# Performance work log

Measured on AMD Instinct MI355X. Metric: run time of the kernel, lower is better.

## Reference

```python
import jax, jax.numpy as jnp
import numpy as np

ALPHA = 0.2       # leakyrelu negative slope
NEG_INF = -9e15   # mask fill value from the torch code
D_OUT = 64


def setup_inputs() -> dict:
    key = jax.random.key(0)
    k1, k2, k3, k4 = jax.random.split(key, 4)
    N, D_IN = 8192, 512
    h = jax.random.normal(k1, (N, D_IN), dtype=jnp.float32)
    W = jax.random.normal(k2, (D_IN, D_OUT), dtype=jnp.float32) * (1.0 / np.sqrt(D_IN))
    a = jax.random.normal(k3, (2 * D_OUT, 1), dtype=jnp.float32) * 0.1
    randomadj = jax.random.randint(k4, (N, N), 0, 2, dtype=jnp.int32)
    return {"h": h, "W": W, "a": a, "randomadj": randomadj}


def reference(h, W, a, randomadj):
    # Wh: [N, D_OUT]
    Wh = h @ W
    # additive attention scores: e[i,j] = leakyrelu(Wh[i]@a1 + Wh[j]@a2)
    Wh1 = Wh @ a[:D_OUT, :]   # [N, 1]
    Wh2 = Wh @ a[D_OUT:, :]   # [N, 1]
    e = jax.nn.leaky_relu(Wh1 + Wh2.T, negative_slope=ALPHA)  # [N, N]
    masked = jnp.where(randomadj > 0, e, NEG_INF)
    attention = jax.nn.softmax(masked, axis=1)  # dropout skipped (eval mode)
    h_prime = attention @ Wh                    # [N, D_OUT]
    return jax.nn.elu(h_prime)                  # concat=True path
```

## Files before the change

kernel.cpp:

```cpp
#include <hip/hip_runtime.h>
#include <stdint.h>


constexpr int NN = 8192;
constexpr int DIN = 512;
constexpr int DOUT = 64;

typedef __attribute__((ext_vector_type(4))) float f32x4;
typedef __attribute__((ext_vector_type(8))) short short8;
typedef int int32x4 __attribute__((ext_vector_type(4)));

__device__ __forceinline__ unsigned short f2bf(float x) {
  union { float f; uint32_t u; } v; v.f = x;
  return (unsigned short)((v.u + 0x7fffu + ((v.u >> 16) & 1u)) >> 16);
}

__device__ __forceinline__ int frag_byte(int c, int d) {
  int g = (c >> 2) & 3;
  int i = (c & 3) | (((c >> 4) & 1) << 2);
  return ((c >> 5) << 12) | ((d >> 4) << 10) | (((g << 4) | (d & 15)) << 4) | (i << 1);
}

__global__ __launch_bounds__(256) void k1_wh(
    const float* __restrict__ h, const float* __restrict__ W,
    const float* __restrict__ a, unsigned short* __restrict__ whb,
    float* __restrict__ wh1, float* __restrict__ wh2) {
  const int t = threadIdx.x, w = t >> 6, l = t & 63;
  const int r = blockIdx.x * 4 + w;
  const int q = l >> 4, cg = l & 15;
  const float* hr = h + (size_t)r * DIN + q * 128;
  const float* Wp = W + (size_t)(q * 128) * DOUT + cg * 4;
  float ax = 0.f, ay = 0.f, az = 0.f, aw = 0.f;
#pragma unroll 4
  for (int kk = 0; kk < 32; ++kk) {
    float4 h4 = *(const float4*)(hr + kk * 4);
    const float* wr = Wp + (size_t)kk * 4 * DOUT;
    float4 w0 = *(const float4*)(wr);
    float4 w1 = *(const float4*)(wr + DOUT);
    float4 w2 = *(const float4*)(wr + 2 * DOUT);
    float4 w3 = *(const float4*)(wr + 3 * DOUT);
    ax = fmaf(h4.x, w0.x, ax); ay = fmaf(h4.x, w0.y, ay); az = fmaf(h4.x, w0.z, az); aw = fmaf(h4.x, w0.w, aw);
    ax = fmaf(h4.y, w1.x, ax); ay = fmaf(h4.y, w1.y, ay); az = fmaf(h4.y, w1.z, az); aw = fmaf(h4.y, w1.w, aw);
    ax = fmaf(h4.z, w2.x, ax); ay = fmaf(h4.z, w2.y, ay); az = fmaf(h4.z, w2.z, az); aw = fmaf(h4.z, w2.w, aw);
    ax = fmaf(h4.w, w3.x, ax); ay = fmaf(h4.w, w3.y, ay); az = fmaf(h4.w, w3.z, az); aw = fmaf(h4.w, w3.w, aw);
  }
  ax += __shfl_xor(ax, 16, 64); ax += __shfl_xor(ax, 32, 64);
  ay += __shfl_xor(ay, 16, 64); ay += __shfl_xor(ay, 32, 64);
  az += __shfl_xor(az, 16, 64); az += __shfl_xor(az, 32, 64);
  aw += __shfl_xor(aw, 16, 64); aw += __shfl_xor(aw, 32, 64);
  float4 a1v = *(const float4*)(a + cg * 4);
  float4 a2v = *(const float4*)(a + DOUT + cg * 4);
  float d1 = ax * a1v.x + ay * a1v.y + az * a1v.z + aw * a1v.w;
  float d2 = ax * a2v.x + ay * a2v.y + az * a2v.z + aw * a2v.w;
#pragma unroll
  for (int m = 8; m >= 1; m >>= 1) { d1 += __shfl_xor(d1, m, 64); d2 += __shfl_xor(d2, m, 64); }
  if (l == 0) { wh1[r] = d1; wh2[r] = d2; }
  if (l < 16) {
    whb[frag_byte(r, cg * 4 + 0) >> 1] = f2bf(ax);
    whb[frag_byte(r, cg * 4 + 1) >> 1] = f2bf(ay);
    whb[frag_byte(r, cg * 4 + 2) >> 1] = f2bf(az);
    whb[frag_byte(r, cg * 4 + 3) >> 1] = f2bf(aw);
  }
}

struct KRegs {
  int32x4 a0, a1;
  float4 f0, f1;
  uint4 v0, v1, v2, v3;
};

__global__ __launch_bounds__(256, 2) void k2_attn(
    const int* __restrict__ adj, const unsigned short* __restrict__ whb,
    const float* __restrict__ wh1, const float* __restrict__ wh2,
    float* __restrict__ out) {
  __shared__ float accs[4][16][64];
  __shared__ float lsum[4][16];
  const int t = threadIdx.x, w = t >> 6, l = t & 63;
  const int r0 = blockIdx.x * 16;
  const int row = l & 15, g = l >> 4;
  const float wh1r = wh1[r0 + row];
  const int jb = w * 2048 + 4 * g;
  const int32x4* adjp = (const int32x4*)(adj + (size_t)(r0 + row) * NN + jb);
  const float4* w2p = (const float4*)(wh2 + jb);
  const uint4* vp = (const uint4*)whb + (size_t)w * 64 * 256 + l;
  f32x4 acc0 = {}, acc1 = {}, acc2 = {}, acc3 = {};
  float lacc = 0.f;

#define LOADC(R, c) do { \
    R.a0 = __builtin_nontemporal_load(adjp + (c) * 8); \
    R.a1 = __builtin_nontemporal_load(adjp + (c) * 8 + 4); \
    R.f0 = w2p[(c) * 8]; R.f1 = w2p[(c) * 8 + 4]; \
    R.v0 = vp[(c) * 256]; R.v1 = vp[(c) * 256 + 64]; \
    R.v2 = vp[(c) * 256 + 128]; R.v3 = vp[(c) * 256 + 192]; \
  } while (0)

#define SC(pv, av, fv) { float s_ = wh1r + (fv); s_ = fmaxf(s_, 0.2f * s_); \
                         float e_ = __expf(s_); pv = ((av) > 0) ? e_ : 0.f; }

#define COMP(R) do { \
    float p0, p1, p2, p3, p4, p5, p6, p7; \
    SC(p0, R.a0.x, R.f0.x) SC(p1, R.a0.y, R.f0.y) SC(p2, R.a0.z, R.f0.z) SC(p3, R.a0.w, R.f0.w) \
    SC(p4, R.a1.x, R.f1.x) SC(p5, R.a1.y, R.f1.y) SC(p6, R.a1.z, R.f1.z) SC(p7, R.a1.w, R.f1.w) \
    lacc += ((p0 + p1) + (p2 + p3)) + ((p4 + p5) + (p6 + p7)); \
    union { uint32_t u[4]; short8 s; } af; \
    af.u[0] = f2bf(p0) | ((uint32_t)f2bf(p1) << 16); \
    af.u[1] = f2bf(p2) | ((uint32_t)f2bf(p3) << 16); \
    af.u[2] = f2bf(p4) | ((uint32_t)f2bf(p5) << 16); \
    af.u[3] = f2bf(p6) | ((uint32_t)f2bf(p7) << 16); \
    union { uint4 q; short8 s; } b0, b1, b2, b3; \
    b0.q = R.v0; b1.q = R.v1; b2.q = R.v2; b3.q = R.v3; \
    acc0 = __builtin_amdgcn_mfma_f32_16x16x32_bf16(af.s, b0.s, acc0, 0, 0, 0); \
    acc1 = __builtin_amdgcn_mfma_f32_16x16x32_bf16(af.s, b1.s, acc1, 0, 0, 0); \
    acc2 = __builtin_amdgcn_mfma_f32_16x16x32_bf16(af.s, b2.s, acc2, 0, 0, 0); \
    acc3 = __builtin_amdgcn_mfma_f32_16x16x32_bf16(af.s, b3.s, acc3, 0, 0, 0); \
  } while (0)

  KRegs A, B;
  LOADC(A, 0);
  LOADC(B, 1);
  for (int c = 0; c + 2 < 64; c += 2) {
    COMP(A); LOADC(A, c + 2);
    COMP(B); LOADC(B, c + 3);
  }
  COMP(A);
  COMP(B);

  lacc += __shfl_xor(lacc, 16, 64);
  lacc += __shfl_xor(lacc, 32, 64);
  if (l < 16) lsum[w][l] = lacc;
  {
    const int rb = (l >> 4) * 4, cl = l & 15;
#define WACC(an, n) { accs[w][rb + 0][(n)*16 + cl] = an[0]; accs[w][rb + 1][(n)*16 + cl] = an[1]; \
                      accs[w][rb + 2][(n)*16 + cl] = an[2]; accs[w][rb + 3][(n)*16 + cl] = an[3]; }
    WACC(acc0, 0) WACC(acc1, 1) WACC(acc2, 2) WACC(acc3, 3)
#undef WACC
  }
  __syncthreads();
  {
    const int rr = t >> 4, dq = (t & 15) * 4;
    float4 s0 = *(const float4*)&accs[0][rr][dq];
    float4 s1 = *(const float4*)&accs[1][rr][dq];
    float4 s2 = *(const float4*)&accs[2][rr][dq];
    float4 s3 = *(const float4*)&accs[3][rr][dq];
    float L = (lsum[0][rr] + lsum[1][rr]) + (lsum[2][rr] + lsum[3][rr]);
    float inv = 1.0f / L;
    float4 o;
    float v;
    v = (s0.x + s1.x + s2.x + s3.x) * inv; o.x = v > 0.f ? v : __expf(v) - 1.f;
    v = (s0.y + s1.y + s2.y + s3.y) * inv; o.y = v > 0.f ? v : __expf(v) - 1.f;
    v = (s0.z + s1.z + s2.z + s3.z) * inv; o.z = v > 0.f ? v : __expf(v) - 1.f;
    v = (s0.w + s1.w + s2.w + s3.w) * inv; o.w = v > 0.f ? v : __expf(v) - 1.f;
    *(float4*)(out + (size_t)(r0 + rr) * DOUT + dq) = o;
  }
#undef LOADC
#undef SC
#undef COMP
}

extern "C" void kernel_launch(void* const* d_in, const int* in_sizes, int n_in,
                              void* d_out, int out_size, void* d_ws, size_t ws_size,
                              hipStream_t stream) {
  const float* h = (const float*)d_in[0];
  const float* W = (const float*)d_in[1];
  const float* a = (const float*)d_in[2];
  const int* adj = (const int*)d_in[3];
  float* out = (float*)d_out;
  char* ws = (char*)d_ws;
  unsigned short* whb = (unsigned short*)ws;
  float* wh1 = (float*)(ws + (1 << 20));
  float* wh2 = (float*)(ws + (1 << 20) + (32 << 10));
  k1_wh<<<NN / 4, 256, 0, stream>>>(h, W, a, whb, wh1, wh2);
  k2_attn<<<NN / 16, 256, 0, stream>>>(adj, whb, wh1, wh2, out);
}
```

Measured before the change: 433.3 us.

## Split attention columns across eight waves and reuse W across rows in projection

The attention kernel now uses 512-thread blocks, with each of 8 waves covering 1024 columns. Launch bounds are raised so more waves stay resident to hide the latency of streaming the adjacency matrix. The projection kernel computes four rows per wave so each W load is reused, and bf16 packing uses the library conversion intrinsic. The cost is more shared memory for the cross-wave reduction, and register pressure under the tighter launch bounds may cause spills.

```diff
diff --git a/kernel.cpp b/kernel.cpp
--- a/kernel.cpp
+++ b/kernel.cpp
@@ -1,4 +1,5 @@
 #include <hip/hip_runtime.h>
+#include <hip/hip_bf16.h>
 #include <stdint.h>
 
 
@@ -26,40 +27,55 @@
     const float* __restrict__ a, unsigned short* __restrict__ whb,
     float* __restrict__ wh1, float* __restrict__ wh2) {
   const int t = threadIdx.x, w = t >> 6, l = t & 63;
-  const int r = blockIdx.x * 4 + w;
+  const int r0 = blockIdx.x * 16 + w * 4;
   const int q = l >> 4, cg = l & 15;
-  const float* hr = h + (size_t)r * DIN + q * 128;
+  const float* h0 = h + (size_t)r0 * DIN + q * 128;
   const float* Wp = W + (size_t)(q * 128) * DOUT + cg * 4;
-  float ax = 0.f, ay = 0.f, az = 0.f, aw = 0.f;
+  f32x4 acc[4] = {};
 #pragma unroll 4
   for (int kk = 0; kk < 32; ++kk) {
-    float4 h4 = *(const float4*)(hr + kk * 4);
     const float* wr = Wp + (size_t)kk * 4 * DOUT;
     float4 w0 = *(const float4*)(wr);
     float4 w1 = *(const float4*)(wr + DOUT);
     float4 w2 = *(const float4*)(wr + 2 * DOUT);
     float4 w3 = *(const float4*)(wr + 3 * DOUT);
-    ax = fmaf(h4.x, w0.x, ax); ay = fmaf(h4.x, w0.y, ay); az = fmaf(h4.x, w0.z, az); aw = fmaf(h4.x, w0.w, aw);
-    ax = fmaf(h4.y, w1.x, ax); ay = fmaf(h4.y, w1.y, ay); az = fmaf(h4.y, w1.z, az); aw = fmaf(h4.y, w1.w, aw);
-    ax = fmaf(h4.z, w2.x, ax); ay = fmaf(h4.z, w2.y, ay); az = fmaf(h4.z, w2.z, az); aw = fmaf(h4.z, w2.w, aw);
-    ax = fmaf(h4.w, w3.x, ax); ay = fmaf(h4.w, w3.y, ay); az = fmaf(h4.w, w3.z, az); aw = fmaf(h4.w, w3.w, aw);
+#pragma unroll
+    for (int r = 0; r < 4; ++r) {
+      float4 h4 = *(const float4*)(h0 + (size_t)r * DIN + kk * 4);
+      acc[r][0] = fmaf(h4.x, w0.x, acc[r][0]); acc[r][1] = fmaf(h4.x, w0.y, acc[r][1]);
+      acc[r][2] = fmaf(h4.x, w0.z, acc[r][2]); acc[r][3] = fmaf(h4.x, w0.w, acc[r][3]);
+      acc[r][0] = fmaf(h4.y, w1.x, acc[r][0]); acc[r][1] = fmaf(h4.y, w1.y, acc[r][1]);
+      acc[r][2] = fmaf(h4.y, w1.z, acc[r][2]); acc[r][3] = fmaf(h4.y, w1.w, acc[r][3]);
+      acc[r][0] = fmaf(h4.z, w2.x, acc[r][0]); acc[r][1] = fmaf(h4.z, w2.y, acc[r][1]);
+      acc[r][2] = fmaf(h4.z, w2.z, acc[r][2]); acc[r][3] = fmaf(h4.z, w2.w, acc[r][3]);
+      acc[r][0] = fmaf(h4.w, w3.x, acc[r][0]); acc[r][1] = fmaf(h4.w, w3.y, acc[r][1]);
+      acc[r][2] = fmaf(h4.w, w3.z, acc[r][2]); acc[r][3] = fmaf(h4.w, w3.w, acc[r][3]);
+    }
   }
-  ax += __shfl_xor(ax, 16, 64); ax += __shfl_xor(ax, 32, 64);
-  ay += __shfl_xor(ay, 16, 64); ay += __shfl_xor(ay, 32, 64);
-  az += __shfl_xor(az, 16, 64); az += __shfl_xor(az, 32, 64);
-  aw += __shfl_xor(aw, 16, 64); aw += __shfl_xor(aw, 32, 64);
+#pragma unroll
+  for (int r = 0; r < 4; ++r)
+#pragma unroll
+    for (int cpt = 0; cpt < 4; ++cpt) {
+      float v = acc[r][cpt];
+      v += __shfl_xor(v, 16, 64);
+      v += __shfl_xor(v, 32, 64);
+      acc[r][cpt] = v;
+    }
   float4 a1v = *(const float4*)(a + cg * 4);
   float4 a2v = *(const float4*)(a + DOUT + cg * 4);
-  float d1 = ax * a1v.x + ay * a1v.y + az * a1v.z + aw * a1v.w;
-  float d2 = ax * a2v.x + ay * a2v.y + az * a2v.z + aw * a2v.w;
 #pragma unroll
-  for (int m = 8; m >= 1; m >>= 1) { d1 += __shfl_xor(d1, m, 64); d2 += __shfl_xor(d2, m, 64); }
-  if (l == 0) { wh1[r] = d1; wh2[r] = d2; }
-  if (l < 16) {
-    whb[frag_byte(r, cg * 4 + 0) >> 1] = f2bf(ax);
-    whb[frag_byte(r, cg * 4 + 1) >> 1] = f2bf(ay);
-    whb[frag_byte(r, cg * 4 + 2) >> 1] = f2bf(az);
-    whb[frag_byte(r, cg * 4 + 3) >> 1] = f2bf(aw);
+  for (int r = 0; r < 4; ++r) {
+    float d1 = acc[r][0] * a1v.x + acc[r][1] * a1v.y + acc[r][2] * a1v.z + acc[r][3] * a1v.w;
+    float d2 = acc[r][0] * a2v.x + acc[r][1] * a2v.y + acc[r][2] * a2v.z + acc[r][3] * a2v.w;
+#pragma unroll
+    for (int m = 8; m >= 1; m >>= 1) { d1 += __shfl_xor(d1, m, 64); d2 += __shfl_xor(d2, m, 64); }
+    if (l == 0) { wh1[r0 + r] = d1; wh2[r0 + r] = d2; }
+    if (l < 16) {
+      whb[frag_byte(r0 + r, cg * 4 + 0) >> 1] = f2bf(acc[r][0]);
+      whb[frag_byte(r0 + r, cg * 4 + 1) >> 1] = f2bf(acc[r][1]);
+      whb[frag_byte(r0 + r, cg * 4 + 2) >> 1] = f2bf(acc[r][2]);
+      whb[frag_byte(r0 + r, cg * 4 + 3) >> 1] = f2bf(acc[r][3]);
+    }
   }
 }
 
@@ -69,20 +85,20 @@
   uint4 v0, v1, v2, v3;
 };
 
-__global__ __launch_bounds__(256, 2) void k2_attn(
+__global__ __launch_bounds__(512, 4) void k2_attn(
     const int* __restrict__ adj, const unsigned short* __restrict__ whb,
     const float* __restrict__ wh1, const float* __restrict__ wh2,
     float* __restrict__ out) {
-  __shared__ float accs[4][16][64];
-  __shared__ float lsum[4][16];
+  __shared__ float accs[8][16][64];
+  __shared__ float lsum[8][16];
   const int t = threadIdx.x, w = t >> 6, l = t & 63;
   const int r0 = blockIdx.x * 16;
   const int row = l & 15, g = l >> 4;
   const float wh1r = wh1[r0 + row];
-  const int jb = w * 2048 + 4 * g;
+  const int jb = w * 1024 + 4 * g;
   const int32x4* adjp = (const int32x4*)(adj + (size_t)(r0 + row) * NN + jb);
   const float4* w2p = (const float4*)(wh2 + jb);
-  const uint4* vp = (const uint4*)whb + (size_t)w * 64 * 256 + l;
+  const uint4* vp = (const uint4*)whb + (size_t)w * 8192 + l;
   f32x4 acc0 = {}, acc1 = {}, acc2 = {}, acc3 = {};
   float lacc = 0.f;
 
@@ -97,16 +113,17 @@
 #define SC(pv, av, fv) { float s_ = wh1r + (fv); s_ = fmaxf(s_, 0.2f * s_); \
                          float e_ = __expf(s_); pv = ((av) > 0) ? e_ : 0.f; }
 
+#define PK2(lo, hi) ({ __hip_bfloat162 b_ = __float22bfloat162_rn(float2{(lo), (hi)}); \
+                       *(uint32_t*)&b_; })
+
 #define COMP(R) do { \
     float p0, p1, p2, p3, p4, p5, p6, p7; \
     SC(p0, R.a0.x, R.f0.x) SC(p1, R.a0.y, R.f0.y) SC(p2, R.a0.z, R.f0.z) SC(p3, R.a0.w, R.f0.w) \
     SC(p4, R.a1.x, R.f1.x) SC(p5, R.a1.y, R.f1.y) SC(p6, R.a1.z, R.f1.z) SC(p7, R.a1.w, R.f1.w) \
     lacc += ((p0 + p1) + (p2 + p3)) + ((p4 + p5) + (p6 + p7)); \
     union { uint32_t u[4]; short8 s; } af; \
-    af.u[0] = f2bf(p0) | ((uint32_t)f2bf(p1) << 16); \
-    af.u[1] = f2bf(p2) | ((uint32_t)f2bf(p3) << 16); \
-    af.u[2] = f2bf(p4) | ((uint32_t)f2bf(p5) << 16); \
-    af.u[3] = f2bf(p6) | ((uint32_t)f2bf(p7) << 16); \
+    af.u[0] = PK2(p0, p1); af.u[1] = PK2(p2, p3); \
+    af.u[2] = PK2(p4, p5); af.u[3] = PK2(p6, p7); \
     union { uint4 q; short8 s; } b0, b1, b2, b3; \
     b0.q = R.v0; b1.q = R.v1; b2.q = R.v2; b3.q = R.v3; \
     acc0 = __builtin_amdgcn_mfma_f32_16x16x32_bf16(af.s, b0.s, acc0, 0, 0, 0); \
@@ -118,7 +135,7 @@
   KRegs A, B;
   LOADC(A, 0);
   LOADC(B, 1);
-  for (int c = 0; c + 2 < 64; c += 2) {
+  for (int c = 0; c + 2 < 32; c += 2) {
     COMP(A); LOADC(A, c + 2);
     COMP(B); LOADC(B, c + 3);
   }
@@ -136,24 +153,27 @@
 #undef WACC
   }
   __syncthreads();
-  {
+  if (t < 256) {
     const int rr = t >> 4, dq = (t & 15) * 4;
-    float4 s0 = *(const float4*)&accs[0][rr][dq];
-    float4 s1 = *(const float4*)&accs[1][rr][dq];
-    float4 s2 = *(const float4*)&accs[2][rr][dq];
-    float4 s3 = *(const float4*)&accs[3][rr][dq];
-    float L = (lsum[0][rr] + lsum[1][rr]) + (lsum[2][rr] + lsum[3][rr]);
+    float sx = 0.f, sy = 0.f, sz = 0.f, sw = 0.f, L = 0.f;
+#pragma unroll
+    for (int ws = 0; ws < 8; ++ws) {
+      float4 sv = *(const float4*)&accs[ws][rr][dq];
+      sx += sv.x; sy += sv.y; sz += sv.z; sw += sv.w;
+      L += lsum[ws][rr];
+    }
     float inv = 1.0f / L;
     float4 o;
     float v;
-    v = (s0.x + s1.x + s2.x + s3.x) * inv; o.x = v > 0.f ? v : __expf(v) - 1.f;
-    v = (s0.y + s1.y + s2.y + s3.y) * inv; o.y = v > 0.f ? v : __expf(v) - 1.f;
-    v = (s0.z + s1.z + s2.z + s3.z) * inv; o.z = v > 0.f ? v : __expf(v) - 1.f;
-    v = (s0.w + s1.w + s2.w + s3.w) * inv; o.w = v > 0.f ? v : __expf(v) - 1.f;
+    v = sx * inv; o.x = v > 0.f ? v : __expf(v) - 1.f;
+    v = sy * inv; o.y = v > 0.f ? v : __expf(v) - 1.f;
+    v = sz * inv; o.z = v > 0.f ? v : __expf(v) - 1.f;
+    v = sw * inv; o.w = v > 0.f ? v : __expf(v) - 1.f;
     *(float4*)(out + (size_t)(r0 + rr) * DOUT + dq) = o;
   }
 #undef LOADC
 #undef SC
+#undef PK2
 #undef COMP
 }
 
@@ -169,6 +189,6 @@
   unsigned short* whb = (unsigned short*)ws;
   float* wh1 = (float*)(ws + (1 << 20));
   float* wh2 = (float*)(ws + (1 << 20) + (32 << 10));
-  k1_wh<<<NN / 4, 256, 0, stream>>>(h, W, a, whb, wh1, wh2);
-  k2_attn<<<NN / 16, 256, 0, stream>>>(adj, whb, wh1, wh2, out);
+  k1_wh<<<NN / 16, 256, 0, stream>>>(h, W, a, whb, wh1, wh2);
+  k2_attn<<<NN / 16, 512, 0, stream>>>(adj, whb, wh1, wh2, out);
 }
```

Result: faster. 423.3 us (-2.3%).
